# Kernel tuning notes

Measured on AMD Instinct MI355X. Metric: run time of the kernel, lower is better.

## Reference

```python
import jax, jax.numpy as jnp
import numpy as np

N, E, C, A, R = 10000, 128000, 128, 10, 8  # nodes, edges, channels, elements, radial basis


def setup_inputs() -> dict:
    key = jax.random.key(0)
    ks = jax.random.split(key, 16)
    inp = {
        'node_attrs': jax.random.uniform(ks[0], (N, A), dtype=jnp.float32),
        'node_feats': jax.random.normal(ks[1], (N, 4 * C), dtype=jnp.float32),
        'edge_attrs': jax.random.normal(ks[2], (E, 4), dtype=jnp.float32),
        'edge_feats': jax.random.normal(ks[3], (E, R), dtype=jnp.float32),
        'edge_index': jax.random.randint(ks[4], (2, E), 0, N, dtype=jnp.int32),
        # linear_up (per-l channel mixing 128->128)
        'W_up0': jax.random.normal(ks[5], (C, C), dtype=jnp.float32),
        'W_up1': jax.random.normal(ks[6], (C, C), dtype=jnp.float32),
        # radial MLP hs=[8,64,64,64,512]
        'R0': jax.random.normal(ks[7], (R, 64), dtype=jnp.float32),
        'R1': jax.random.normal(ks[8], (64, 64), dtype=jnp.float32),
        'R2': jax.random.normal(ks[9], (64, 64), dtype=jnp.float32),
        'R3': jax.random.normal(ks[10], (64, 4 * C), dtype=jnp.float32),
        # density net hs=[8,1]
        'W_density': jax.random.normal(ks[11], (R, 1), dtype=jnp.float32),
        # linear: irreps_mid (256x0e+256x1o) -> target (128x0e+128x1o)
        'W_lin0': jax.random.normal(ks[12], (2 * C, C), dtype=jnp.float32),
        'W_lin1': jax.random.normal(ks[13], (2 * C, C), dtype=jnp.float32),
        # skip_tp: FullyConnectedTP(node_feats, node_attrs(scalars)) -> hidden
        'W_skip0': jax.random.normal(ks[14], (C, A, C), dtype=jnp.float32),
        'W_skip1': jax.random.normal(ks[15], (C, A, C), dtype=jnp.float32),
    }
    return inp


def reference(node_attrs, node_feats, edge_attrs, edge_feats, edge_index,
              W_up0, W_up1, R0, R1, R2, R3, W_density, W_lin0, W_lin1,
              W_skip0, W_skip1):
    n = node_feats.shape[0]
    silu = jax.nn.silu
    x0 = node_feats[:, :C]                       # [N,128]  l=0
    x1 = node_feats[:, C:].reshape(n, C, 3)      # [N,128,3] l=1

    # skip_tp (node_attrs are scalars -> per-element channel mixing)
    norm_skip = 1.0 / np.sqrt(C * A)
    sc0 = jnp.einsum('nu,na,uav->nv', x0, node_attrs, W_skip0) * norm_skip
    sc1 = jnp.einsum('nuk,na,uav->nvk', x1, node_attrs, W_skip1) * norm_skip
    sc = jnp.concatenate([sc0, sc1.reshape(n, 3 * C)], axis=1)  # [N,512]

    # linear_up
    h0 = (x0 @ W_up0) / np.sqrt(C)
    h1 = jnp.einsum('nuk,uv->nvk', x1, W_up1) / np.sqrt(C)

    # radial MLP -> per-edge TP weights [E, 4*C]
    w = silu((edge_feats @ R0) / np.sqrt(R))
    w = silu((w @ R1) / np.sqrt(64))
    w = silu((w @ R2) / np.sqrt(64))
    w = (w @ R3) / np.sqrt(64)
    w1, w2, w3, w4 = jnp.split(w, 4, axis=1)     # each [E,128]

    # edge density
    edge_density = jnp.tanh(((edge_feats @ W_density) / np.sqrt(R)) ** 2)  # [E,1]

    sender = edge_index[0]
    receiver = edge_index[1]
    density = jax.ops.segment_sum(edge_density, receiver, num_segments=n)  # [N,1]

    # gather sender features
    hs0 = h0[sender]   # [E,128]
    hs1 = h1[sender]   # [E,128,3]
    y0 = edge_attrs[:, :1]   # [E,1]
    y1 = edge_attrs[:, 1:4]  # [E,3]

    # uvu tensor product paths (edge_irreps x edge_attrs -> irreps_mid)
    m0a = w1 * hs0 * y0                                      # 0e x 0e -> 0e
    m0b = w4 * jnp.einsum('euk,ek->eu', hs1, y1) / np.sqrt(3.0)  # 1o x 1o -> 0e
    m1a = (w2 * hs0)[:, :, None] * y1[:, None, :]            # 0e x 1o -> 1o
    m1b = w3[:, :, None] * hs1 * y0[:, :, None]              # 1o x 0e -> 1o

    mid0 = jnp.concatenate([m0a, m0b], axis=1)               # [E,256]
    mid1 = jnp.concatenate([m1a, m1b], axis=1)               # [E,256,3]

    # scatter messages to receivers
    M0 = jax.ops.segment_sum(mid0, receiver, num_segments=n)                     # [N,256]
    M1 = jax.ops.segment_sum(mid1.reshape(-1, 2 * C * 3), receiver, num_segments=n).reshape(n, 2 * C, 3)

    # linear irreps_mid -> target, then density normalization
    denom = density + 1.0
    out0 = (M0 @ W_lin0) / np.sqrt(2 * C) / denom                               # [N,128]
    out1 = jnp.einsum('nuk,uv->nvk', M1, W_lin1) / np.sqrt(2 * C) / denom[:, :, None]

    # reshape_irreps: [N, channels, sum(2l+1)] = [N,128,4]
    message = jnp.concatenate([out0[:, :, None], out1], axis=2)
    return message, sc
```

## Files before the change

kernel.cpp:

```cpp
#include <hip/hip_runtime.h>
#include <hip/hip_bf16.h>
#include <hip/hip_fp16.h>

#define N_NODES 10000
#define N_EDGES 128000
constexpr int C = 128;
constexpr int A = 10;

constexpr float INV_SQRT_C  = 0.08838834764831845f;
constexpr float INV_SQRT_R  = 0.35355339059327373f;
constexpr float INV_SQRT_64 = 0.125f;
constexpr float INV_SQRT_CA = 0.027950849718747374f;
constexpr float INV_SQRT_2C = 0.0625f;
constexpr float INV_SQRT_3  = 0.57735026918962576f;

typedef short short8 __attribute__((ext_vector_type(8)));
typedef _Float16 f16x8 __attribute__((ext_vector_type(8)));
typedef _Float16 f16x2 __attribute__((ext_vector_type(2)));
typedef float f32x4 __attribute__((ext_vector_type(4)));

__device__ __forceinline__ float silu_f(float x) { return x / (1.0f + __expf(-x)); }

__device__ __forceinline__ void atomic_add_f32(float* p, float v) {
  __hip_atomic_fetch_add(p, v, __ATOMIC_RELAXED, __HIP_MEMORY_SCOPE_AGENT);
}

__device__ __forceinline__ unsigned short f2h(float f) {
  return __builtin_bit_cast(unsigned short, (_Float16)f);
}

__device__ __forceinline__ unsigned int pk2h(float a, float b) {
  auto h = __builtin_amdgcn_cvt_pkrtz(a, b);
  return __builtin_bit_cast(unsigned int, h);
}

__device__ __forceinline__ unsigned int pkmul_h2(unsigned int x, unsigned int y) {
  const f16x2 a = __builtin_bit_cast(f16x2, x), b = __builtin_bit_cast(f16x2, y);
  return __builtin_bit_cast(unsigned int, a * b);
}

__device__ __forceinline__ float4 h4tof4(uint2 v) {
  const __half2 lo = __builtin_bit_cast(__half2, v.x);
  const __half2 hi = __builtin_bit_cast(__half2, v.y);
  const float2 flo = __half22float2(lo), fhi = __half22float2(hi);
  return make_float4(flo.x, flo.y, fhi.x, fhi.y);
}

__device__ __forceinline__ void cvtw(const float* __restrict__ src,
                                     unsigned short* __restrict__ dst,
                                     int idx, int lgN, int KT) {
  const int k = idx >> lgN;
  const int n = idx & ((1 << lgN) - 1);
  dst[((n * KT + (k >> 5)) << 5) + (k & 31)] = f2h(src[idx]);
}

__global__ __launch_bounds__(256) void k_prep_node(
    const float* __restrict__ nf, const float* __restrict__ Wu0,
    const float* __restrict__ Wu1, __half* __restrict__ Hh,
    const float* __restrict__ W0, const float* __restrict__ W1,
    unsigned short* __restrict__ B0, unsigned short* __restrict__ B1,
    const float* __restrict__ R1, unsigned short* __restrict__ R1a,
    const float* __restrict__ R2, unsigned short* __restrict__ R2a,
    const float* __restrict__ R3, unsigned short* __restrict__ R3a,
    const int* __restrict__ eidx, int* __restrict__ counts) {
  __shared__ __align__(16) float xs[8][C][4];
  const int bid = blockIdx.x, t = threadIdx.x;
  if (bid < 1250) {
    const int n0 = bid * 8;
    for (int idx = t; idx < 8 * 512; idx += 256) {
      const int nn = idx >> 9, q = idx & 511;
      const float val = nf[(size_t)(n0 + nn) * 512 + q];
      if (q < C) xs[nn][q][0] = val;
      else { const int r = q - C; xs[nn][r / 3][1 + r % 3] = val; }
    }
    __syncthreads();
    const int g = t >> 7, v = t & 127;
    float acc[4][4] = {};
    for (int u = 0; u < C; ++u) {
      const float w0 = Wu0[u * C + v];
      const float w1 = Wu1[u * C + v];
#pragma unroll
      for (int nn = 0; nn < 4; ++nn) {
        const float4 xv = *(const float4*)&xs[g * 4 + nn][u][0];
        acc[nn][0] = fmaf(xv.x, w0, acc[nn][0]);
        acc[nn][1] = fmaf(xv.y, w1, acc[nn][1]);
        acc[nn][2] = fmaf(xv.z, w1, acc[nn][2]);
        acc[nn][3] = fmaf(xv.w, w1, acc[nn][3]);
      }
    }
#pragma unroll
    for (int nn = 0; nn < 4; ++nn) {
      const int n = n0 + g * 4 + nn;
      uint2 o;
      o.x = pk2h(acc[nn][0] * INV_SQRT_C, acc[nn][1] * INV_SQRT_C);
      o.y = pk2h(acc[nn][2] * INV_SQRT_C, acc[nn][3] * INV_SQRT_C);
      *(uint2*)&Hh[(size_t)n * 512 + v * 4] = o;
    }
  } else {
    const int b = bid - 1250;
    if (b < 640) {
      const int idx = b * 256 + t;
      const int k = idx >> 7, col = idx & 127;
      const int u = k / 10, a = k - u * 10;
      const int kp = a * 128 + u;
      const int dst = ((kp >> 5) * 128 + col) * 32 + (kp & 31);
      B0[dst] = f2h(W0[idx]);
      B1[dst] = f2h(W1[idx]);
    } else if (b < 656) {
      cvtw(R1, R1a, (b - 640) * 256 + t, 6, 2);
    } else if (b < 672) {
      cvtw(R2, R2a, (b - 656) * 256 + t, 6, 2);
    } else if (b < 800) {
      cvtw(R3, R3a, (b - 672) * 256 + t, 9, 2);
    } else {
      const int e = (b - 800) * 256 + t;
      if (e < N_EDGES) atomicAdd(&counts[eidx[N_EDGES + e]], 1);
    }
  }
}

__global__ __launch_bounds__(256) void k_skip_mfma(
    const float* __restrict__ nf, const float* __restrict__ attrs,
    const unsigned short* __restrict__ B0, const unsigned short* __restrict__ B1,
    float* __restrict__ out_sc) {
  __shared__ __align__(16) unsigned short xs[64][136];
  __shared__ float at[64][10];
  __shared__ __align__(16) unsigned short zs[2][2][64][40];

  const int t = threadIdx.x;
  const int wave = t >> 6, lane = t & 63;
  const bool isG0 = blockIdx.x < 157;
  const int r0 = isG0 ? blockIdx.x * 64 : (blockIdx.x - 157) * 64;
  const int rcount = isG0 ? 10000 : 30000;
  const unsigned short* __restrict__ Bsw = isG0 ? B0 : B1;

  for (int idx = t; idx < 64 * 128; idx += 256) {
    const int i = idx >> 7, u = idx & 127;
    const int r = r0 + i;
    float v = 0.f;
    if (r < rcount) {
      if (isG0) v = nf[(size_t)r * 512 + u];
      else {
        const int n = r / 3, kc = r - n * 3;
        v = nf[(size_t)n * 512 + 128 + u * 3 + kc];
      }
    }
    xs[i][u] = f2h(v);
  }
  for (int idx = t; idx < 640; idx += 256) {
    const int i = idx / 10, a = idx - (idx / 10) * 10;
    const int r = r0 + i;
    float v = 0.f;
    if (r < rcount) v = attrs[(size_t)(isG0 ? r : r / 3) * 10 + a];
    at[i][a] = v;
  }
  __syncthreads();

  const int m = lane & 15, q = lane >> 4;
  const int colB = wave * 32;
  const int rr = t >> 2;
  const int off = (t & 3) * 8;

  unsigned int atr2[10];
#pragma unroll
  for (int a = 0; a < 10; ++a) {
    const unsigned int h = f2h(at[rr][a]);
    atr2[a] = h | (h << 16);
  }

  f32x4 acc[4][2];
#pragma unroll
  for (int rt = 0; rt < 4; ++rt)
#pragma unroll
    for (int ct = 0; ct < 2; ++ct) acc[rt][ct] = (f32x4){0.f, 0.f, 0.f, 0.f};

  f16x8 bf[2][2];
#pragma unroll
  for (int sub = 0; sub < 2; ++sub)
#pragma unroll
    for (int ct = 0; ct < 2; ++ct)
      bf[sub][ct] = *(const f16x8*)&Bsw[(size_t)(sub * 128 + colB + ct * 16 + m) * 32 + q * 8];

#pragma unroll
  for (int a = 0; a < 10; ++a) {
    const unsigned int av2 = atr2[a];
#pragma unroll
    for (int pp = 0; pp < 2; ++pp) {
      const int p = a * 2 + pp;
      const int buf = p & 1;
#pragma unroll
      for (int sub = 0; sub < 2; ++sub) {
        const int kk = 2 * pp + sub;
        const uint4 xv = *(const uint4*)&xs[rr][kk * 32 + off];
        uint4 z;
        z.x = pkmul_h2(xv.x, av2);
        z.y = pkmul_h2(xv.y, av2);
        z.z = pkmul_h2(xv.z, av2);
        z.w = pkmul_h2(xv.w, av2);
        *(uint4*)&zs[buf][sub][rr][off] = z;
      }
      __syncthreads();

      f16x8 bfn[2][2];
      if (p < 19) {
        const int ktn = (p + 1) * 2;
#pragma unroll
        for (int sub = 0; sub < 2; ++sub)
#pragma unroll
          for (int ct = 0; ct < 2; ++ct)
            bfn[sub][ct] = *(const f16x8*)&Bsw[(size_t)((ktn + sub) * 128 + colB + ct * 16 + m) * 32 + q * 8];
      }

#pragma unroll
      for (int sub = 0; sub < 2; ++sub) {
#pragma unroll
        for (int rt = 0; rt < 4; ++rt) {
          const f16x8 afrag = *(const f16x8*)&zs[buf][sub][rt * 16 + m][q * 8];
#pragma unroll
          for (int ct = 0; ct < 2; ++ct)
            acc[rt][ct] = __builtin_amdgcn_mfma_f32_16x16x32_f16(
                afrag, bf[sub][ct], acc[rt][ct], 0, 0, 0);
        }
      }
      bf[0][0] = bfn[0][0]; bf[0][1] = bfn[0][1];
      bf[1][0] = bfn[1][0]; bf[1][1] = bfn[1][1];
    }
  }

#pragma unroll
  for (int rt = 0; rt < 4; ++rt) {
#pragma unroll
    for (int reg = 0; reg < 4; ++reg) {
      const int rloc = rt * 16 + q * 4 + reg;
      const int r = r0 + rloc;
      if (r < rcount) {
#pragma unroll
        for (int ct = 0; ct < 2; ++ct) {
          const int v = colB + ct * 16 + m;
          const float val = acc[rt][ct][reg] * INV_SQRT_CA;
          if (isG0) {
            out_sc[(size_t)r * 512 + v] = val;
          } else {
            const int n = r / 3, kc = r - (r / 3) * 3;
            out_sc[(size_t)n * 512 + 128 + v * 3 + kc] = val;
          }
        }
      }
    }
  }
}

__global__ __launch_bounds__(1024) void k_scan(const int* __restrict__ counts,
                                               int* __restrict__ offsets,
                                               int* __restrict__ cursor) {
  __shared__ int part[1024];
  const int t = threadIdx.x;
  int local[10];
  int s = 0;
#pragma unroll
  for (int i = 0; i < 10; ++i) {
    const int idx = t * 10 + i;
    const int c = (idx < N_NODES) ? counts[idx] : 0;
    local[i] = s;
    s += c;
  }
  part[t] = s;
  __syncthreads();
  for (int off = 1; off < 1024; off <<= 1) {
    const int add = (t >= off) ? part[t - off] : 0;
    __syncthreads();
    part[t] += add;
    __syncthreads();
  }
  const int pre = (t > 0) ? part[t - 1] : 0;
#pragma unroll
  for (int i = 0; i < 10; ++i) {
    const int idx = t * 10 + i;
    if (idx < N_NODES) {
      const int o = pre + local[i];
      offsets[idx] = o;
      cursor[idx] = o;
    }
  }
  if (t == 1023) offsets[N_NODES] = part[1023];
}

__global__ __launch_bounds__(256) void k_scatter(
    const int* __restrict__ eidx, const float* __restrict__ ea_g,
    const float* __restrict__ ef_g,
    int* __restrict__ cursor,
    int* __restrict__ snd_s, int* __restrict__ rcv_s,
    float* __restrict__ ea_s, float* __restrict__ ef_s) {
  const int e = blockIdx.x * 256 + threadIdx.x;
  if (e < N_EDGES) {
    const int r = eidx[N_EDGES + e];
    const int pos = atomicAdd(&cursor[r], 1);
    snd_s[pos] = eidx[e];
    rcv_s[pos] = r;
    ((float4*)ea_s)[pos] = ((const float4*)ea_g)[e];
    ((float4*)ef_s)[pos * 2]     = ((const float4*)ef_g)[e * 2];
    ((float4*)ef_s)[pos * 2 + 1] = ((const float4*)ef_g)[e * 2 + 1];
  }
}

__global__ __launch_bounds__(256, 4) void k_mlp_msg(
    const float* __restrict__ ef_s, const float* __restrict__ ea_s,
    const int* __restrict__ snd_s, const int* __restrict__ rcv_s,
    const int* __restrict__ offsets,
    const float* __restrict__ R0, const unsigned short* __restrict__ R1a,
    const unsigned short* __restrict__ R2a, const unsigned short* __restrict__ R3a,
    const float* __restrict__ Wd, const __half* __restrict__ Hh,
    float* __restrict__ M, float* __restrict__ density) {
  __shared__ __align__(16) unsigned short actA[128][72];
  __shared__ __align__(16) unsigned char uni[18432];
  __shared__ __align__(16) float ys[128][4];
  __shared__ __align__(16) int sn[144];
  __shared__ __align__(16) int rc[128];
  float (*efs)[9] = (float (*)[9]) & uni[0];
  unsigned short (*actB)[72] = (unsigned short (*)[72]) & uni[0];
  __half (*wls2)[536] = (__half (*)[536]) & uni[0];

  const int t = threadIdx.x;
  const int wave = t >> 6, lane = t & 63, m = lane & 15, q = lane >> 4;
  const int e0 = blockIdx.x * 128;

  {
    const float4 v = *(const float4*)&ef_s[(size_t)e0 * 8 + t * 4];
    const int e = t >> 1, c0 = (t & 1) * 4;
    efs[e][c0] = v.x; efs[e][c0 + 1] = v.y;
    efs[e][c0 + 2] = v.z; efs[e][c0 + 3] = v.w;
  }
  if (t < 128) {
    *(float4*)&ys[t][0] = ((const float4*)ea_s)[e0 + t];
    sn[t] = snd_s[e0 + t];
    rc[t] = rcv_s[e0 + t];
  } else if (t < 144) {
    sn[t] = 0;
  }
  __syncthreads();

  const int u = t & 127, half = t >> 7;
  const size_t ucol = (size_t)(u << 2);
  uint2 hA[4], hB[4];
#pragma unroll
  for (int j = 0; j < 4; ++j)
    hA[j] = *(const uint2*)&Hh[(size_t)sn[j] * 512 + ucol];
#pragma unroll
  for (int j = 0; j < 4; ++j)
    hB[j] = *(const uint2*)&Hh[(size_t)sn[4 + j] * 512 + ucol];

  if (t < 128) {
    float s = 0.f;
#pragma unroll
    for (int i = 0; i < 8; ++i) s = fmaf(efs[t][i], Wd[i], s);
    s *= INV_SQRT_R;
    atomic_add_f32(&density[rc[t]], tanhf(s * s));
  }

  {
    const int e = t & 127, j0 = (t >> 7) * 32;
    float a[32] = {};
#pragma unroll
    for (int i = 0; i < 8; ++i) {
      const float v = efs[e][i];
#pragma unroll
      for (int jj = 0; jj < 32; ++jj)
        a[jj] = fmaf(v, R0[i * 64 + j0 + jj], a[jj]);
    }
#pragma unroll
    for (int g = 0; g < 8; ++g) {
      uint2 pk;
      pk.x = pk2h(silu_f(a[4 * g] * INV_SQRT_R), silu_f(a[4 * g + 1] * INV_SQRT_R));
      pk.y = pk2h(silu_f(a[4 * g + 2] * INV_SQRT_R), silu_f(a[4 * g + 3] * INV_SQRT_R));
      *(uint2*)&actA[e][j0 + g * 4] = pk;
    }
  }
  __syncthreads();

  {
    const f16x8 af0 = *(const f16x8*)&R1a[(((wave * 16 + m) * 2 + 0) << 5) + q * 8];
    const f16x8 af1 = *(const f16x8*)&R1a[(((wave * 16 + m) * 2 + 1) << 5) + q * 8];
#pragma unroll
    for (int et = 0; et < 8; ++et) {
      const f16x8 bf0 = *(const f16x8*)&actA[et * 16 + m][q * 8];
      const f16x8 bf1 = *(const f16x8*)&actA[et * 16 + m][32 + q * 8];
      f32x4 c = {0.f, 0.f, 0.f, 0.f};
      c = __builtin_amdgcn_mfma_f32_16x16x32_f16(af0, bf0, c, 0, 0, 0);
      c = __builtin_amdgcn_mfma_f32_16x16x32_f16(af1, bf1, c, 0, 0, 0);
      uint2 pk;
      pk.x = pk2h(silu_f(c[0] * INV_SQRT_64), silu_f(c[1] * INV_SQRT_64));
      pk.y = pk2h(silu_f(c[2] * INV_SQRT_64), silu_f(c[3] * INV_SQRT_64));
      *(uint2*)&actB[et * 16 + m][wave * 16 + q * 4] = pk;
    }
  }
  __syncthreads();

  {
    const f16x8 af0 = *(const f16x8*)&R2a[(((wave * 16 + m) * 2 + 0) << 5) + q * 8];
    const f16x8 af1 = *(const f16x8*)&R2a[(((wave * 16 + m) * 2 + 1) << 5) + q * 8];
#pragma unroll
    for (int et = 0; et < 8; ++et) {
      const f16x8 bf0 = *(const f16x8*)&actB[et * 16 + m][q * 8];
      const f16x8 bf1 = *(const f16x8*)&actB[et * 16 + m][32 + q * 8];
      f32x4 c = {0.f, 0.f, 0.f, 0.f};
      c = __builtin_amdgcn_mfma_f32_16x16x32_f16(af0, bf0, c, 0, 0, 0);
      c = __builtin_amdgcn_mfma_f32_16x16x32_f16(af1, bf1, c, 0, 0, 0);
      uint2 pk;
      pk.x = pk2h(silu_f(c[0] * INV_SQRT_64), silu_f(c[1] * INV_SQRT_64));
      pk.y = pk2h(silu_f(c[2] * INV_SQRT_64), silu_f(c[3] * INV_SQRT_64));
      *(uint2*)&actA[et * 16 + m][wave * 16 + q * 4] = pk;
    }
  }
  __syncthreads();

  const int baseJ = (wave & 1) * 4 + (wave >> 1) * 16;
  f16x8 afL[4][2], afH[4][2];
#pragma unroll
  for (int i = 0; i < 4; ++i) {
#pragma unroll
    for (int kt = 0; kt < 2; ++kt) {
      const int JL = baseJ + i, JH = JL + 8;
      afL[i][kt] = *(const f16x8*)&R3a[(((JL * 16 + m) * 2 + kt) << 5) + q * 8];
      afH[i][kt] = *(const f16x8*)&R3a[(((JH * 16 + m) * 2 + kt) << 5) + q * 8];
    }
  }

  float a0 = 0.f, a1 = 0.f, a2 = 0.f, a3 = 0.f;
  int cur = rc[0];
  int s0c = offsets[cur], s1c = offsets[cur + 1];
  const int colx = (half ? 128 + u : u) * 2;

  auto flush = [&](int n, int s0, int s1) {
    float* Mp = &M[(size_t)n * 1024 + (half << 9) + (u << 2)];
    if (s0 >= e0 && s1 <= e0 + 128) {
      *(float4*)Mp = make_float4(a0, a1, a2, a3);
    } else {
      atomic_add_f32(Mp + 0, a0);
      atomic_add_f32(Mp + 1, a1);
      atomic_add_f32(Mp + 2, a2);
      atomic_add_f32(Mp + 3, a3);
    }
  };

  auto proc = [&](const uint2 hcur, unsigned int pr, const float4 yv, int n) {
    if (n != cur) {
      flush(cur, s0c, s1c);
      a0 = a1 = a2 = a3 = 0.f;
      cur = n;
      s0c = offsets[n];
      s1c = offsets[n + 1];
    }
    const float4 h4 = h4tof4(hcur);
    const __half2 ph = __builtin_bit_cast(__half2, pr);
    const float2 pw = __half22float2(ph);
    if (half == 0) {
      a0 = fmaf(pw.x * h4.x, yv.x, a0);
      const float c1 = pw.y * h4.x;
      a1 = fmaf(c1, yv.y, a1);
      a2 = fmaf(c1, yv.z, a2);
      a3 = fmaf(c1, yv.w, a3);
    } else {
      const float dt = h4.y * yv.y + h4.z * yv.z + h4.w * yv.w;
      a0 = fmaf(pw.y * dt, INV_SQRT_3, a0);
      const float c3 = pw.x * yv.x;
      a1 = fmaf(c3, h4.y, a1);
      a2 = fmaf(c3, h4.z, a2);
      a3 = fmaf(c3, h4.w, a3);
    }
  };

#define MSG_GROUP(G, HX)                                                    \
  {                                                                         \
    const int gb = ch * 16 + (G) * 4;                                       \
    unsigned int prv[4];                                                    \
    float4 yv4[4];                                                          \
    _Pragma("unroll") for (int j = 0; j < 4; ++j)                           \
        prv[j] = *(const unsigned int*)&wls2[(G) * 4 + j][colx];            \
    _Pragma("unroll") for (int j = 0; j < 4; ++j)                           \
        yv4[j] = *(const float4*)&ys[gb + j][0];                            \
    const int4 rc4 = *(const int4*)&rc[gb];                                 \
    proc(HX[0], prv[0], yv4[0], rc4.x);                                     \
    proc(HX[1], prv[1], yv4[1], rc4.y);                                     \
    proc(HX[2], prv[2], yv4[2], rc4.z);                                     \
    proc(HX[3], prv[3], yv4[3], rc4.w);                                     \
    const int4 sn4 = *(const int4*)&sn[gb + 8];                             \
    HX[0] = *(const uint2*)&Hh[(size_t)sn4.x * 512 + ucol];                 \
    HX[1] = *(const uint2*)&Hh[(size_t)sn4.y * 512 + ucol];                 \
    HX[2] = *(const uint2*)&Hh[(size_t)sn4.z * 512 + ucol];                 \
    HX[3] = *(const uint2*)&Hh[(size_t)sn4.w * 512 + ucol];                 \
  }

#pragma unroll 1
  for (int ch = 0; ch < 8; ++ch) {
    {
      const f16x8 bf0 = *(const f16x8*)&actA[ch * 16 + m][q * 8];
      const f16x8 bf1 = *(const f16x8*)&actA[ch * 16 + m][32 + q * 8];
#pragma unroll
      for (int i = 0; i < 4; ++i) {
        f32x4 cL = {0.f, 0.f, 0.f, 0.f}, cH = {0.f, 0.f, 0.f, 0.f};
        cL = __builtin_amdgcn_mfma_f32_16x16x32_f16(afL[i][0], bf0, cL, 0, 0, 0);
        cL = __builtin_amdgcn_mfma_f32_16x16x32_f16(afL[i][1], bf1, cL, 0, 0, 0);
        cH = __builtin_amdgcn_mfma_f32_16x16x32_f16(afH[i][0], bf0, cH, 0, 0, 0);
        cH = __builtin_amdgcn_mfma_f32_16x16x32_f16(afH[i][1], bf1, cH, 0, 0, 0);
        uint4 pk;
        pk.x = pk2h(cL[0] * INV_SQRT_64, cH[0] * INV_SQRT_64);
        pk.y = pk2h(cL[1] * INV_SQRT_64, cH[1] * INV_SQRT_64);
        pk.z = pk2h(cL[2] * INV_SQRT_64, cH[2] * INV_SQRT_64);
        pk.w = pk2h(cL[3] * INV_SQRT_64, cH[3] * INV_SQRT_64);
        const int JL = baseJ + i;
        const int pidx0 = ((JL < 8) ? JL * 16 : (JL - 16) * 16 + 128) + q * 4;
        *(uint4*)&wls2[m][pidx0 * 2] = pk;
      }
    }
    MSG_GROUP(0, hA)
    MSG_GROUP(1, hB)
    MSG_GROUP(2, hA)
    MSG_GROUP(3, hB)
  }
#undef MSG_GROUP
  flush(cur, s0c, s1c);
}

__global__ __launch_bounds__(256) void k_out(
    const float* __restrict__ M, const float* __restrict__ density,
    const float* __restrict__ Wl0, const float* __restrict__ Wl1,
    float* __restrict__ out) {
  __shared__ __align__(16) float Ms[8][256][4];
  __shared__ float dens[8];
  const int t = threadIdx.x;
  const int n0 = blockIdx.x * 8;
  const float4* Msrc = (const float4*)&M[(size_t)n0 * 1024];
  float4* Mdst = (float4*)&Ms[0][0][0];
  for (int idx = t; idx < 8 * 256; idx += 256) Mdst[idx] = Msrc[idx];
  if (t < 8) dens[t] = density[n0 + t] + 1.0f;
  __syncthreads();
  const int g = t >> 7, v = t & 127;
  float acc[4][4] = {};
  for (int p0 = 0; p0 < 256; p0 += 4) {
    float4 mv[4][4];
#pragma unroll
    for (int nn = 0; nn < 4; ++nn)
#pragma unroll
      for (int j = 0; j < 4; ++j)
        mv[nn][j] = *(const float4*)&Ms[g * 4 + nn][p0 + j][0];
#pragma unroll
    for (int j = 0; j < 4; ++j) {
      const float w0 = Wl0[(p0 + j) * C + v];
      const float w1 = Wl1[(p0 + j) * C + v];
#pragma unroll
      for (int nn = 0; nn < 4; ++nn) {
        acc[nn][0] = fmaf(mv[nn][j].x, w0, acc[nn][0]);
        acc[nn][1] = fmaf(mv[nn][j].y, w1, acc[nn][1]);
        acc[nn][2] = fmaf(mv[nn][j].z, w1, acc[nn][2]);
        acc[nn][3] = fmaf(mv[nn][j].w, w1, acc[nn][3]);
      }
    }
  }
#pragma unroll
  for (int nn = 0; nn < 4; ++nn) {
    const int n = n0 + g * 4 + nn;
    const float sc = INV_SQRT_2C / dens[g * 4 + nn];
    float4 o;
    o.x = acc[nn][0] * sc; o.y = acc[nn][1] * sc;
    o.z = acc[nn][2] * sc; o.w = acc[nn][3] * sc;
    *(float4*)&out[(size_t)n * 512 + v * 4] = o;
  }
}

extern "C" void kernel_launch(void* const* d_in, const int* in_sizes, int n_in,
                              void* d_out, int out_size, void* d_ws, size_t ws_size,
                              hipStream_t stream) {
  const float* node_attrs = (const float*)d_in[0];
  const float* node_feats = (const float*)d_in[1];
  const float* edge_attrs = (const float*)d_in[2];
  const float* edge_feats = (const float*)d_in[3];
  const int*   edge_index = (const int*)d_in[4];
  const float* W_up0 = (const float*)d_in[5];
  const float* W_up1 = (const float*)d_in[6];
  const float* R0 = (const float*)d_in[7];
  const float* R1 = (const float*)d_in[8];
  const float* R2 = (const float*)d_in[9];
  const float* R3 = (const float*)d_in[10];
  const float* Wd  = (const float*)d_in[11];
  const float* Wl0 = (const float*)d_in[12];
  const float* Wl1 = (const float*)d_in[13];
  const float* Ws0 = (const float*)d_in[14];
  const float* Ws1 = (const float*)d_in[15];
  float* out = (float*)d_out;

  __half* Hh = (__half*)d_ws;
  float* M = (float*)d_ws + (size_t)N_NODES * 512;
  float* density = M + (size_t)N_NODES * 1024;
  int* counts  = (int*)(density + 10000);
  int* offsets = counts + 10016;
  int* cursor  = offsets + 10016;
  int* snd_s   = cursor + 10016;
  int* rcv_s   = snd_s + N_EDGES;
  float* ea_s  = (float*)(rcv_s + N_EDGES);
  unsigned short* Bsw0 = (unsigned short*)(ea_s + (size_t)N_EDGES * 4);
  unsigned short* Bsw1 = Bsw0 + 1280 * 128;
  unsigned short* R1a  = Bsw1 + 1280 * 128;
  unsigned short* R2a  = R1a + 64 * 64;
  unsigned short* R3a  = R2a + 64 * 64;
  float* ef_s  = (float*)(R3a + 64 * 512);

  hipMemsetAsync(M, 0, ((size_t)N_NODES * 1024 + 10000 + 10016) * sizeof(float),
                 stream);

  k_prep_node<<<2550, 256, 0, stream>>>(node_feats, W_up0, W_up1, Hh, Ws0, Ws1,
                                        Bsw0, Bsw1, R1, R1a, R2, R2a, R3, R3a,
                                        edge_index, counts);
  k_scan<<<1, 1024, 0, stream>>>(counts, offsets, cursor);
  k_scatter<<<(N_EDGES + 255) / 256, 256, 0, stream>>>(
      edge_index, edge_attrs, edge_feats, cursor, snd_s, rcv_s, ea_s, ef_s);
  k_mlp_msg<<<N_EDGES / 128, 256, 0, stream>>>(ef_s, ea_s, snd_s, rcv_s,
                                               offsets, R0, R1a, R2a, R3a, Wd,
                                               Hh, M, density);
  k_out<<<N_NODES / 8, 256, 0, stream>>>(M, density, Wl0, Wl1, out);
  k_skip_mfma<<<157 + 469, 256, 0, stream>>>(node_feats, node_attrs, Bsw0, Bsw1,
                                             out + (size_t)N_NODES * 512);
}
```

Measured before the change: 318.9 us.

## Move node linear_up and output linear onto fp16 MFMA kernels

Replaces the scalar-FMA linear_up (in the node prep kernel) and the scalar-FMA output linear with MFMA 16x16x32 fp16 kernels. The weights are pre-converted to fp16 and swizzled in the prep kernel, and activations are cast to fp16 and staged in LDS. The aim is to cut FP32 ALU time in these two dense GEMM stages. In exchange it adds fp16 rounding of the M aggregates and inputs, plus one extra kernel launch.

```diff
diff --git a/kernel.cpp b/kernel.cpp
--- a/kernel.cpp
+++ b/kernel.cpp
@@ -54,68 +54,123 @@
   dst[((n * KT + (k >> 5)) << 5) + (k & 31)] = f2h(src[idx]);
 }
 
-__global__ __launch_bounds__(256) void k_prep_node(
-    const float* __restrict__ nf, const float* __restrict__ Wu0,
-    const float* __restrict__ Wu1, __half* __restrict__ Hh,
+__global__ __launch_bounds__(256) void k_prep(
     const float* __restrict__ W0, const float* __restrict__ W1,
     unsigned short* __restrict__ B0, unsigned short* __restrict__ B1,
     const float* __restrict__ R1, unsigned short* __restrict__ R1a,
     const float* __restrict__ R2, unsigned short* __restrict__ R2a,
     const float* __restrict__ R3, unsigned short* __restrict__ R3a,
+    const float* __restrict__ Wu0, unsigned short* __restrict__ Wua0,
+    const float* __restrict__ Wu1, unsigned short* __restrict__ Wua1,
+    const float* __restrict__ Wl0, unsigned short* __restrict__ Wla0,
+    const float* __restrict__ Wl1, unsigned short* __restrict__ Wla1,
     const int* __restrict__ eidx, int* __restrict__ counts) {
-  __shared__ __align__(16) float xs[8][C][4];
-  const int bid = blockIdx.x, t = threadIdx.x;
-  if (bid < 1250) {
-    const int n0 = bid * 8;
-    for (int idx = t; idx < 8 * 512; idx += 256) {
-      const int nn = idx >> 9, q = idx & 511;
-      const float val = nf[(size_t)(n0 + nn) * 512 + q];
-      if (q < C) xs[nn][q][0] = val;
-      else { const int r = q - C; xs[nn][r / 3][1 + r % 3] = val; }
-    }
-    __syncthreads();
-    const int g = t >> 7, v = t & 127;
-    float acc[4][4] = {};
-    for (int u = 0; u < C; ++u) {
-      const float w0 = Wu0[u * C + v];
-      const float w1 = Wu1[u * C + v];
-#pragma unroll
-      for (int nn = 0; nn < 4; ++nn) {
-        const float4 xv = *(const float4*)&xs[g * 4 + nn][u][0];
-        acc[nn][0] = fmaf(xv.x, w0, acc[nn][0]);
-        acc[nn][1] = fmaf(xv.y, w1, acc[nn][1]);
-        acc[nn][2] = fmaf(xv.z, w1, acc[nn][2]);
-        acc[nn][3] = fmaf(xv.w, w1, acc[nn][3]);
-      }
-    }
-#pragma unroll
-    for (int nn = 0; nn < 4; ++nn) {
-      const int n = n0 + g * 4 + nn;
-      uint2 o;
-      o.x = pk2h(acc[nn][0] * INV_SQRT_C, acc[nn][1] * INV_SQRT_C);
-      o.y = pk2h(acc[nn][2] * INV_SQRT_C, acc[nn][3] * INV_SQRT_C);
-      *(uint2*)&Hh[(size_t)n * 512 + v * 4] = o;
-    }
+  const int b = blockIdx.x, t = threadIdx.x;
+  if (b < 640) {
+    const int idx = b * 256 + t;
+    const int k = idx >> 7, col = idx & 127;
+    const int u = k / 10, a = k - u * 10;
+    const int kp = a * 128 + u;
+    const int dst = ((kp >> 5) * 128 + col) * 32 + (kp & 31);
+    B0[dst] = f2h(W0[idx]);
+    B1[dst] = f2h(W1[idx]);
+  } else if (b < 656) {
+    cvtw(R1, R1a, (b - 640) * 256 + t, 6, 2);
+  } else if (b < 672) {
+    cvtw(R2, R2a, (b - 656) * 256 + t, 6, 2);
+  } else if (b < 800) {
+    cvtw(R3, R3a, (b - 672) * 256 + t, 9, 2);
+  } else if (b < 864) {
+    cvtw(Wu0, Wua0, (b - 800) * 256 + t, 7, 4);
+  } else if (b < 928) {
+    cvtw(Wu1, Wua1, (b - 864) * 256 + t, 7, 4);
+  } else if (b < 1056) {
+    cvtw(Wl0, Wla0, (b - 928) * 256 + t, 7, 8);
+  } else if (b < 1184) {
+    cvtw(Wl1, Wla1, (b - 1056) * 256 + t, 7, 8);
   } else {
-    const int b = bid - 1250;
-    if (b < 640) {
-      const int idx = b * 256 + t;
-      const int k = idx >> 7, col = idx & 127;
-      const int u = k / 10, a = k - u * 10;
-      const int kp = a * 128 + u;
-      const int dst = ((kp >> 5) * 128 + col) * 32 + (kp & 31);
-      B0[dst] = f2h(W0[idx]);
-      B1[dst] = f2h(W1[idx]);
-    } else if (b < 656) {
-      cvtw(R1, R1a, (b - 640) * 256 + t, 6, 2);
-    } else if (b < 672) {
-      cvtw(R2, R2a, (b - 656) * 256 + t, 6, 2);
-    } else if (b < 800) {
-      cvtw(R3, R3a, (b - 672) * 256 + t, 9, 2);
+    const int e = (b - 1184) * 256 + t;
+    if (e < N_EDGES) atomicAdd(&counts[eidx[N_EDGES + e]], 1);
+  }
+}
+
+__global__ __launch_bounds__(256) void k_node_mfma(
+    const float* __restrict__ nf, const unsigned short* __restrict__ Wua0,
+    const unsigned short* __restrict__ Wua1, __half* __restrict__ Hh) {
+  __shared__ __align__(16) unsigned short xs[64][136];
+  __shared__ __align__(16) unsigned short hst[16][512];
+  const int t = threadIdx.x;
+  const int wave = t >> 6, lane = t & 63, m = lane & 15, q = lane >> 4;
+  const int n0 = blockIdx.x * 16;
+
+  for (int i = t; i < 2048; i += 256) {
+    const int nn = i >> 7, qq = (i & 127) * 4;
+    const float4 v = *(const float4*)&nf[(size_t)(n0 + nn) * 512 + qq];
+    const float vals[4] = {v.x, v.y, v.z, v.w};
+    if (qq < 128) {
+#pragma unroll
+      for (int j = 0; j < 4; ++j) xs[nn][qq + j] = f2h(vals[j]);
     } else {
-      const int e = (b - 800) * 256 + t;
-      if (e < N_EDGES) atomicAdd(&counts[eidx[N_EDGES + e]], 1);
-    }
+#pragma unroll
+      for (int j = 0; j < 4; ++j) {
+        const int r = qq + j - 128;
+        const int u = r / 3, kc = r - u * 3;
+        xs[16 + nn * 3 + kc][u] = f2h(vals[j]);
+      }
+    }
+  }
+  __syncthreads();
+
+  const int colB = wave * 32;
+  f32x4 acc[4][2];
+#pragma unroll
+  for (int rt = 0; rt < 4; ++rt)
+#pragma unroll
+    for (int ct = 0; ct < 2; ++ct) acc[rt][ct] = (f32x4){0.f, 0.f, 0.f, 0.f};
+
+#pragma unroll
+  for (int kt = 0; kt < 4; ++kt) {
+    f16x8 bf0[2], bf1[2];
+#pragma unroll
+    for (int ct = 0; ct < 2; ++ct) {
+      const int col = colB + ct * 16 + m;
+      bf0[ct] = *(const f16x8*)&Wua0[((col * 4 + kt) << 5) + q * 8];
+      bf1[ct] = *(const f16x8*)&Wua1[((col * 4 + kt) << 5) + q * 8];
+    }
+#pragma unroll
+    for (int rt = 0; rt < 4; ++rt) {
+      const f16x8 af = *(const f16x8*)&xs[rt * 16 + m][kt * 32 + q * 8];
+#pragma unroll
+      for (int ct = 0; ct < 2; ++ct)
+        acc[rt][ct] = __builtin_amdgcn_mfma_f32_16x16x32_f16(
+            af, rt == 0 ? bf0[ct] : bf1[ct], acc[rt][ct], 0, 0, 0);
+    }
+  }
+
+#pragma unroll
+  for (int rt = 0; rt < 4; ++rt) {
+#pragma unroll
+    for (int reg = 0; reg < 4; ++reg) {
+      const int rloc = rt * 16 + q * 4 + reg;
+#pragma unroll
+      for (int ct = 0; ct < 2; ++ct) {
+        const int v = colB + ct * 16 + m;
+        const unsigned short hv = f2h(acc[rt][ct][reg] * INV_SQRT_C);
+        if (rt == 0) {
+          hst[rloc][v * 4] = hv;
+        } else {
+          const int rr = rloc - 16;
+          const int nn = rr / 3, kc = rr - nn * 3;
+          hst[nn][v * 4 + 1 + kc] = hv;
+        }
+      }
+    }
+  }
+  __syncthreads();
+  for (int i = t; i < 2048; i += 256) {
+    const int nn = i >> 7, pos = i & 127;
+    *(uint2*)&Hh[(size_t)(n0 + nn) * 512 + pos * 4] =
+        *(const uint2*)&hst[nn][pos * 4];
   }
 }
 
@@ -521,49 +576,82 @@
   flush(cur, s0c, s1c);
 }
 
-__global__ __launch_bounds__(256) void k_out(
+__global__ __launch_bounds__(256) void k_out_mfma(
     const float* __restrict__ M, const float* __restrict__ density,
-    const float* __restrict__ Wl0, const float* __restrict__ Wl1,
-    float* __restrict__ out) {
-  __shared__ __align__(16) float Ms[8][256][4];
-  __shared__ float dens[8];
+    const unsigned short* __restrict__ Wla0,
+    const unsigned short* __restrict__ Wla1, float* __restrict__ out) {
+  __shared__ __align__(16) unsigned char sm[64 * 264 * 2];
+  __shared__ float dens[16];
+  unsigned short (*xso)[264] = (unsigned short (*)[264])sm;
+  float (*ost)[512] = (float (*)[512])sm;
   const int t = threadIdx.x;
-  const int n0 = blockIdx.x * 8;
-  const float4* Msrc = (const float4*)&M[(size_t)n0 * 1024];
-  float4* Mdst = (float4*)&Ms[0][0][0];
-  for (int idx = t; idx < 8 * 256; idx += 256) Mdst[idx] = Msrc[idx];
-  if (t < 8) dens[t] = density[n0 + t] + 1.0f;
-  __syncthreads();
-  const int g = t >> 7, v = t & 127;
-  float acc[4][4] = {};
-  for (int p0 = 0; p0 < 256; p0 += 4) {
-    float4 mv[4][4];
-#pragma unroll
-    for (int nn = 0; nn < 4; ++nn)
-#pragma unroll
-      for (int j = 0; j < 4; ++j)
-        mv[nn][j] = *(const float4*)&Ms[g * 4 + nn][p0 + j][0];
-#pragma unroll
-    for (int j = 0; j < 4; ++j) {
-      const float w0 = Wl0[(p0 + j) * C + v];
-      const float w1 = Wl1[(p0 + j) * C + v];
-#pragma unroll
-      for (int nn = 0; nn < 4; ++nn) {
-        acc[nn][0] = fmaf(mv[nn][j].x, w0, acc[nn][0]);
-        acc[nn][1] = fmaf(mv[nn][j].y, w1, acc[nn][1]);
-        acc[nn][2] = fmaf(mv[nn][j].z, w1, acc[nn][2]);
-        acc[nn][3] = fmaf(mv[nn][j].w, w1, acc[nn][3]);
-      }
-    }
-  }
-#pragma unroll
-  for (int nn = 0; nn < 4; ++nn) {
-    const int n = n0 + g * 4 + nn;
-    const float sc = INV_SQRT_2C / dens[g * 4 + nn];
-    float4 o;
-    o.x = acc[nn][0] * sc; o.y = acc[nn][1] * sc;
-    o.z = acc[nn][2] * sc; o.w = acc[nn][3] * sc;
-    *(float4*)&out[(size_t)n * 512 + v * 4] = o;
+  const int wave = t >> 6, lane = t & 63, m = lane & 15, q = lane >> 4;
+  const int n0 = blockIdx.x * 16;
+
+  if (t < 16) dens[t] = INV_SQRT_2C / (density[n0 + t] + 1.0f);
+
+  const float4* Mf4 = (const float4*)&M[(size_t)n0 * 1024];
+  for (int i = t; i < 4096; i += 256) {
+    const float4 v = Mf4[i];
+    const int nn = i >> 8, p = i & 255;
+    xso[nn][p] = f2h(v.x);
+    const int rb = 16 + nn * 3;
+    xso[rb][p] = f2h(v.y);
+    xso[rb + 1][p] = f2h(v.z);
+    xso[rb + 2][p] = f2h(v.w);
+  }
+  __syncthreads();
+
+  const int colB = wave * 32;
+  f32x4 acc[4][2];
+#pragma unroll
+  for (int rt = 0; rt < 4; ++rt)
+#pragma unroll
+    for (int ct = 0; ct < 2; ++ct) acc[rt][ct] = (f32x4){0.f, 0.f, 0.f, 0.f};
+
+#pragma unroll
+  for (int kt = 0; kt < 8; ++kt) {
+    f16x8 bf0[2], bf1[2];
+#pragma unroll
+    for (int ct = 0; ct < 2; ++ct) {
+      const int col = colB + ct * 16 + m;
+      bf0[ct] = *(const f16x8*)&Wla0[((col * 8 + kt) << 5) + q * 8];
+      bf1[ct] = *(const f16x8*)&Wla1[((col * 8 + kt) << 5) + q * 8];
+    }
+#pragma unroll
+    for (int rt = 0; rt < 4; ++rt) {
+      const f16x8 af = *(const f16x8*)&xso[rt * 16 + m][kt * 32 + q * 8];
+#pragma unroll
+      for (int ct = 0; ct < 2; ++ct)
+        acc[rt][ct] = __builtin_amdgcn_mfma_f32_16x16x32_f16(
+            af, rt == 0 ? bf0[ct] : bf1[ct], acc[rt][ct], 0, 0, 0);
+    }
+  }
+  __syncthreads();
+
+#pragma unroll
+  for (int rt = 0; rt < 4; ++rt) {
+#pragma unroll
+    for (int reg = 0; reg < 4; ++reg) {
+      const int rloc = rt * 16 + q * 4 + reg;
+#pragma unroll
+      for (int ct = 0; ct < 2; ++ct) {
+        const int v = colB + ct * 16 + m;
+        if (rt == 0) {
+          ost[rloc][v * 4] = acc[rt][ct][reg] * dens[rloc];
+        } else {
+          const int rr = rloc - 16;
+          const int nn = rr / 3, kc = rr - nn * 3;
+          ost[nn][v * 4 + 1 + kc] = acc[rt][ct][reg] * dens[nn];
+        }
+      }
+    }
+  }
+  __syncthreads();
+  for (int i = t; i < 2048; i += 256) {
+    const int nn = i >> 7, pos = i & 127;
+    *(float4*)&out[(size_t)(n0 + nn) * 512 + pos * 4] =
+        *(const float4*)&ost[nn][pos * 4];
   }
 }
 
@@ -602,21 +690,26 @@
   unsigned short* R1a  = Bsw1 + 1280 * 128;
   unsigned short* R2a  = R1a + 64 * 64;
   unsigned short* R3a  = R2a + 64 * 64;
-  float* ef_s  = (float*)(R3a + 64 * 512);
+  unsigned short* Wua0 = R3a + 64 * 512;
+  unsigned short* Wua1 = Wua0 + 128 * 128;
+  unsigned short* Wla0 = Wua1 + 128 * 128;
+  unsigned short* Wla1 = Wla0 + 256 * 128;
+  float* ef_s  = (float*)(Wla1 + 256 * 128);
 
   hipMemsetAsync(M, 0, ((size_t)N_NODES * 1024 + 10000 + 10016) * sizeof(float),
                  stream);
 
-  k_prep_node<<<2550, 256, 0, stream>>>(node_feats, W_up0, W_up1, Hh, Ws0, Ws1,
-                                        Bsw0, Bsw1, R1, R1a, R2, R2a, R3, R3a,
-                                        edge_index, counts);
+  k_prep<<<1684, 256, 0, stream>>>(Ws0, Ws1, Bsw0, Bsw1, R1, R1a, R2, R2a, R3,
+                                   R3a, W_up0, Wua0, W_up1, Wua1, Wl0, Wla0,
+                                   Wl1, Wla1, edge_index, counts);
+  k_node_mfma<<<N_NODES / 16, 256, 0, stream>>>(node_feats, Wua0, Wua1, Hh);
   k_scan<<<1, 1024, 0, stream>>>(counts, offsets, cursor);
   k_scatter<<<(N_EDGES + 255) / 256, 256, 0, stream>>>(
       edge_index, edge_attrs, edge_feats, cursor, snd_s, rcv_s, ea_s, ef_s);
   k_mlp_msg<<<N_EDGES / 128, 256, 0, stream>>>(ef_s, ea_s, snd_s, rcv_s,
                                                offsets, R0, R1a, R2a, R3a, Wd,
                                                Hh, M, density);
-  k_out<<<N_NODES / 8, 256, 0, stream>>>(M, density, Wl0, Wl1, out);
+  k_out_mfma<<<N_NODES / 16, 256, 0, stream>>>(M, density, Wla0, Wla1, out);
   k_skip_mfma<<<157 + 469, 256, 0, stream>>>(node_feats, node_attrs, Bsw0, Bsw1,
                                              out + (size_t)N_NODES * 512);
 }
```

Result: faster. 278.2 us (-12.8%).
